# Kernel optimization log

Measured on AMD Instinct MI355X. Metric: run time of the kernel, lower is better.

The kernel has to match this reference:

```python
import jax, jax.numpy as jnp
import numpy as np

# ---- dims (mirror reconstructed HybridSignToTextModel) ----
INPUT_SIZE = 256
CONV_CH = 512
ENC_HID = 512          # per-direction encoder GRU hidden
ENC_OUT = 2 * ENC_HID  # bidirectional concat = 1024
DEC_LAYERS = 2
DEC_HID = 512
EMB = 512
VOCAB = 8000
ATTN = 512
MAX_DEC = 50
SOS, EOS, PAD = 1, 2, 0


def _gru_cell(x, h, Wih, Whh, bih, bhh):
    # torch GRUCell math. x:(B,I) h:(B,H) Wih:(3H,I) Whh:(3H,H)
    gi = x @ Wih.T + bih
    gh = h @ Whh.T + bhh
    H = h.shape[-1]
    ir, iz, inn = gi[:, :H], gi[:, H:2*H], gi[:, 2*H:]
    hr, hz, hn = gh[:, :H], gh[:, H:2*H], gh[:, 2*H:]
    r = jax.nn.sigmoid(ir + hr)
    z = jax.nn.sigmoid(iz + hz)
    n = jnp.tanh(inn + r * hn)
    return (1.0 - z) * n + z * h


def _gru_layer(xs, h0, Wih, Whh, bih, bhh, reverse=False):
    # xs: (T,B,I) -> outputs (T,B,H), final h (B,H)
    def step(h, x):
        h = _gru_cell(x, h, Wih, Whh, bih, bhh)
        return h, h
    hT, ys = jax.lax.scan(step, h0, xs, reverse=reverse)
    return ys, hT


def _conv1d(x, w, b, stride):
    # x:(B,C,T) w:(O,C,K) 'same'-ish padding K//2
    k = w.shape[-1]
    y = jax.lax.conv_general_dilated(x, w, (stride,), [(k // 2, k // 2)],
                                     dimension_numbers=("NCH", "OIH", "NCH"))
    return y + b[None, :, None]


def setup_inputs() -> dict:
    key = jax.random.key(0)
    ks = iter(jax.random.split(key, 40))
    def rn(shape, s=0.05):
        return (jax.random.normal(next(ks), shape, dtype=jnp.float32) * s)
    p = {}
    p["features"] = jax.random.normal(next(ks), (32, 512, INPUT_SIZE), dtype=jnp.float32)
    # conv encoder: 2 conv1d layers, stride 2 each, ReLU
    p["conv_w1"] = rn((CONV_CH, INPUT_SIZE, 5)); p["conv_b1"] = rn((CONV_CH,))
    p["conv_w2"] = rn((CONV_CH, CONV_CH, 5)); p["conv_b2"] = rn((CONV_CH,))
    # bidirectional encoder GRU (1 layer)
    for d in ("f", "b"):
        p[f"enc_Wih_{d}"] = rn((3 * ENC_HID, CONV_CH))
        p[f"enc_Whh_{d}"] = rn((3 * ENC_HID, ENC_HID))
        p[f"enc_bih_{d}"] = rn((3 * ENC_HID,))
        p[f"enc_bhh_{d}"] = rn((3 * ENC_HID,))
    # hidden bridge: 2*ENC_HID -> DEC_LAYERS*DEC_HID
    p["bridge_W"] = rn((DEC_LAYERS * DEC_HID, 2 * ENC_HID)); p["bridge_b"] = rn((DEC_LAYERS * DEC_HID,))
    # decoder embedding
    p["emb"] = rn((VOCAB, EMB), 0.1)
    # Bahdanau attention
    p["attn_We"] = rn((ATTN, ENC_OUT)); p["attn_Wd"] = rn((ATTN, DEC_HID)); p["attn_v"] = rn((ATTN,))
    # decoder GRU: 2 layers; layer0 in = EMB+ENC_OUT, layer1 in = DEC_HID
    ins = [EMB + ENC_OUT, DEC_HID]
    for l in range(DEC_LAYERS):
        p[f"dec_Wih{l}"] = rn((3 * DEC_HID, ins[l]))
        p[f"dec_Whh{l}"] = rn((3 * DEC_HID, DEC_HID))
        p[f"dec_bih{l}"] = rn((3 * DEC_HID,))
        p[f"dec_bhh{l}"] = rn((3 * DEC_HID,))
    # output proj: DEC_HID + ENC_OUT -> VOCAB
    p["proj_W"] = rn((VOCAB, DEC_HID + ENC_OUT)); p["proj_b"] = rn((VOCAB,))
    return p


def reference(features, conv_w1, conv_b1, conv_w2, conv_b2,
              enc_Wih_f, enc_Whh_f, enc_bih_f, enc_bhh_f,
              enc_Wih_b, enc_Whh_b, enc_bih_b, enc_bhh_b,
              bridge_W, bridge_b, emb, attn_We, attn_Wd, attn_v,
              dec_Wih0, dec_Whh0, dec_bih0, dec_bhh0,
              dec_Wih1, dec_Whh1, dec_bih1, dec_bhh1,
              proj_W, proj_b):
    B = features.shape[0]
    # ---- conv encoder ----
    x = features.transpose(0, 2, 1)                 # (B,C,T)
    x = jax.nn.relu(_conv1d(x, conv_w1, conv_b1, 2))
    x = jax.nn.relu(_conv1d(x, conv_w2, conv_b2, 2))
    x = x.transpose(2, 0, 1)                        # (T',B,C)
    # ---- bidirectional GRU encoder ----
    h0 = jnp.zeros((B, ENC_HID), features.dtype)
    yf, hf = _gru_layer(x, h0, enc_Wih_f, enc_Whh_f, enc_bih_f, enc_bhh_f)
    yb, hb = _gru_layer(x, h0, enc_Wih_b, enc_Whh_b, enc_bih_b, enc_bhh_b, reverse=True)
    enc_out = jnp.concatenate([yf, yb], -1).transpose(1, 0, 2)   # (B,T',2H)
    combined = jnp.concatenate([hf, hb], -1)                      # (B,2H)
    dec_h = (combined @ bridge_W.T + bridge_b).reshape(B, DEC_LAYERS, DEC_HID).transpose(1, 0, 2)
    # precompute attention keys
    enc_proj = jnp.einsum("bte,ae->bta", enc_out, attn_We)       # (B,T',A)

    def attention(h_top):
        score = jnp.einsum("bta,a->bt", jnp.tanh(enc_proj + (h_top @ attn_Wd.T)[:, None, :]), attn_v)
        w = jax.nn.softmax(score, axis=-1)
        return jnp.einsum("bt,bte->be", w, enc_out)               # (B,2H)

    def decode_step(carry, _):
        tok, h = carry                                            # h: (L,B,H)
        e = emb[tok]                                              # (B,EMB)
        ctx = attention(h[-1])
        g0 = _gru_cell(jnp.concatenate([e, ctx], -1), h[0], dec_Wih0, dec_Whh0, dec_bih0, dec_bhh0)
        g1 = _gru_cell(g0, h[1], dec_Wih1, dec_Whh1, dec_bih1, dec_bhh1)
        logits = jnp.concatenate([g1, ctx], -1) @ proj_W.T + proj_b
        nxt = jnp.argmax(logits, -1)
        return (nxt, jnp.stack([g0, g1])), nxt

    init_tok = jnp.full((B,), SOS, dtype=jnp.int32)
    _, toks = jax.lax.scan(decode_step, (init_tok, dec_h), None, length=MAX_DEC - 1)
    decoded = jnp.concatenate([init_tok[:, None], toks.T], axis=1)  # (B,MAX_DEC)
    return decoded
```

## Files before the change

### kernel.cpp

```cpp
#include <hip/hip_runtime.h>
#include <math.h>

#define DINLINE __device__ __forceinline__

DINLINE float sigmoidf_(float x) { return 1.f / (1.f + expf(-x)); }

__device__ __align__(256) float g_ws[36200000];

__global__ void im2col1_kernel(const float* __restrict__ feat, float* __restrict__ P) {
  size_t i = (size_t)blockIdx.x * 256 + threadIdx.x;
  int col = (int)(i % 1280);
  int row = (int)(i / 1280);
  int c = col / 5, k = col - c * 5;
  int l = row & 255, b = row >> 8;
  int pos = 2 * l + k - 2;
  P[i] = (pos >= 0 && pos < 512) ? feat[((size_t)b * 512 + pos) * 256 + c] : 0.f;
}

__global__ void im2col2_kernel(const float* __restrict__ y1, float* __restrict__ P) {
  size_t i = (size_t)blockIdx.x * 256 + threadIdx.x;
  int col = (int)(i % 2560);
  int row = (int)(i / 2560);
  int c = col / 5, k = col - c * 5;
  int l = row & 127, b = row >> 7;
  int pos = 2 * l + k - 2;
  P[i] = (pos >= 0 && pos < 256) ? y1[((size_t)b * 256 + pos) * 512 + c] : 0.f;
}

__global__ __launch_bounds__(256) void sgemm128(
    const float* __restrict__ A, const float* __restrict__ B,
    const float* __restrict__ bias, float* __restrict__ C,
    int M, int N, int K, int relu) {
  __shared__ float As[8][132];
  __shared__ float Bs[8][132];
  int bm = blockIdx.y * 128, bn = blockIdx.x * 128;
  int tid = threadIdx.x;
  int tx = tid & 15, ty = tid >> 4;
  float acc[8][8];
#pragma unroll
  for (int i = 0; i < 8; ++i)
#pragma unroll
    for (int j = 0; j < 8; ++j) acc[i][j] = 0.f;
  int lr = tid >> 1;
  int lc = (tid & 1) * 4;
  const float* Arow = A + (size_t)(bm + lr) * K + lc;
  const float* Brow = B + (size_t)(bn + lr) * K + lc;
  for (int k0 = 0; k0 < K; k0 += 8) {
    float4 av = *(const float4*)(Arow + k0);
    float4 bv = *(const float4*)(Brow + k0);
    As[lc + 0][lr] = av.x; As[lc + 1][lr] = av.y; As[lc + 2][lr] = av.z; As[lc + 3][lr] = av.w;
    Bs[lc + 0][lr] = bv.x; Bs[lc + 1][lr] = bv.y; Bs[lc + 2][lr] = bv.z; Bs[lc + 3][lr] = bv.w;
    __syncthreads();
#pragma unroll
    for (int kk = 0; kk < 8; ++kk) {
      float4 a0 = *(const float4*)&As[kk][ty * 8];
      float4 a1 = *(const float4*)&As[kk][ty * 8 + 4];
      float4 b0 = *(const float4*)&Bs[kk][tx * 8];
      float4 b1 = *(const float4*)&Bs[kk][tx * 8 + 4];
      float aa[8] = {a0.x, a0.y, a0.z, a0.w, a1.x, a1.y, a1.z, a1.w};
      float bb[8] = {b0.x, b0.y, b0.z, b0.w, b1.x, b1.y, b1.z, b1.w};
#pragma unroll
      for (int i = 0; i < 8; ++i)
#pragma unroll
        for (int j = 0; j < 8; ++j) acc[i][j] += aa[i] * bb[j];
    }
    __syncthreads();
  }
#pragma unroll
  for (int i = 0; i < 8; ++i) {
    int m = bm + ty * 8 + i;
#pragma unroll
    for (int j = 0; j < 8; ++j) {
      int n = bn + tx * 8 + j;
      float v = acc[i][j] + (bias ? bias[n] : 0.f);
      if (relu) v = fmaxf(v, 0.f);
      C[(size_t)m * N + n] = v;
    }
  }
}

__global__ __launch_bounds__(256) void enc_gru_step(
    const float* __restrict__ gi_f, const float* __restrict__ gi_b,
    const float* __restrict__ Whh_f, const float* __restrict__ bhh_f,
    const float* __restrict__ Whh_b, const float* __restrict__ bhh_b,
    const float* __restrict__ h_in, float* __restrict__ h_out,
    float* __restrict__ enc_out, int s) {
  int dir = blockIdx.x >> 6;
  int j = ((blockIdx.x & 63) << 3) + (threadIdx.x >> 5);
  int b = threadIdx.x & 31;
  __shared__ float4 hs4[32 * 128];
  const float4* hbase = (const float4*)(h_in + dir * 32 * 512);
  for (int i = threadIdx.x; i < 32 * 128; i += 256) {
    int bb = i >> 7, kf = i & 127;
    hs4[bb * 128 + (kf ^ (bb & 7))] = hbase[i];
  }
  __syncthreads();
  const float* gi = dir ? gi_b : gi_f;
  const float* Whh = dir ? Whh_b : Whh_f;
  const float* bhh = dir ? bhh_b : bhh_f;
  int t = dir ? (127 - s) : s;
  const float4* wr = (const float4*)(Whh + (size_t)j * 512);
  const float4* wz = (const float4*)(Whh + (size_t)(512 + j) * 512);
  const float4* wn = (const float4*)(Whh + (size_t)(1024 + j) * 512);
  const float4* hrow = hs4 + b * 128;
  int sw = b & 7;
  float sr = 0.f, sz = 0.f, sn = 0.f;
#pragma unroll 4
  for (int kf = 0; kf < 128; ++kf) {
    float4 hv = hrow[kf ^ sw];
    float4 r4 = wr[kf];
    float4 z4 = wz[kf];
    float4 n4 = wn[kf];
    sr += hv.x * r4.x + hv.y * r4.y + hv.z * r4.z + hv.w * r4.w;
    sz += hv.x * z4.x + hv.y * z4.y + hv.z * z4.z + hv.w * z4.w;
    sn += hv.x * n4.x + hv.y * n4.y + hv.z * n4.z + hv.w * n4.w;
  }
  const float* g = gi + ((size_t)b * 128 + t) * 1536;
  float r = sigmoidf_(g[j] + sr + bhh[j]);
  float z = sigmoidf_(g[512 + j] + sz + bhh[512 + j]);
  float n = tanhf(g[1024 + j] + r * (sn + bhh[1024 + j]));
  float4 hj4 = hrow[(j >> 2) ^ sw];
  float hj = ((const float*)&hj4)[j & 3];
  float hnew = (1.f - z) * n + z * hj;
  h_out[dir * 32 * 512 + b * 512 + j] = hnew;
  enc_out[((size_t)b * 128 + t) * 1024 + dir * 512 + j] = hnew;
}

__global__ __launch_bounds__(256) void dec_gru_step(
    const float* __restrict__ gi, const float* __restrict__ Whh,
    const float* __restrict__ bhh,
    const float* __restrict__ h_in, float* __restrict__ h_out) {
  int j = (blockIdx.x << 3) + (threadIdx.x >> 5);
  int b = threadIdx.x & 31;
  __shared__ float4 hs4[32 * 128];
  const float4* hbase = (const float4*)h_in;
  for (int i = threadIdx.x; i < 32 * 128; i += 256) {
    int bb = i >> 7, kf = i & 127;
    hs4[bb * 128 + (kf ^ (bb & 7))] = hbase[i];
  }
  __syncthreads();
  const float4* wr = (const float4*)(Whh + (size_t)j * 512);
  const float4* wz = (const float4*)(Whh + (size_t)(512 + j) * 512);
  const float4* wn = (const float4*)(Whh + (size_t)(1024 + j) * 512);
  const float4* hrow = hs4 + b * 128;
  int sw = b & 7;
  float sr = 0.f, sz = 0.f, sn = 0.f;
#pragma unroll 4
  for (int kf = 0; kf < 128; ++kf) {
    float4 hv = hrow[kf ^ sw];
    float4 r4 = wr[kf];
    float4 z4 = wz[kf];
    float4 n4 = wn[kf];
    sr += hv.x * r4.x + hv.y * r4.y + hv.z * r4.z + hv.w * r4.w;
    sz += hv.x * z4.x + hv.y * z4.y + hv.z * z4.z + hv.w * z4.w;
    sn += hv.x * n4.x + hv.y * n4.y + hv.z * n4.z + hv.w * n4.w;
  }
  const float* g = gi + (size_t)b * 1536;
  float r = sigmoidf_(g[j] + sr + bhh[j]);
  float z = sigmoidf_(g[512 + j] + sz + bhh[512 + j]);
  float n = tanhf(g[1024 + j] + r * (sn + bhh[1024 + j]));
  float4 hj4 = hrow[(j >> 2) ^ sw];
  float hj = ((const float*)&hj4)[j & 3];
  h_out[b * 512 + j] = (1.f - z) * n + z * hj;
}

__global__ __launch_bounds__(256) void gemvB(
    const float* __restrict__ A1, const int* __restrict__ tokidx, int len1,
    const float* __restrict__ A2, int len2,
    const float* __restrict__ W, const float* __restrict__ bias,
    float* __restrict__ out0, float* __restrict__ out1, int split, int N, int K) {
  int tid = threadIdx.x;
  int s = tid & 7, nl = tid >> 3;
  int n = blockIdx.x * 32 + nl;
  __shared__ float4 xs4[32 * 32];
  float acc[32];
#pragma unroll
  for (int b = 0; b < 32; ++b) acc[b] = 0.f;
  const float4* W4 = (const float4*)(W + (size_t)n * K);
  int K4 = K >> 2;
  int len1_4 = len1 >> 2;
  for (int k0 = 0; k0 < K4; k0 += 32) {
    __syncthreads();
    for (int idx = tid; idx < 1024; idx += 256) {
      int b = idx >> 5, kf = idx & 31;
      int gk = k0 + kf;
      float4 v;
      if (gk < len1_4) {
        const float* src = tokidx ? (A1 + (size_t)tokidx[b] * len1) : (A1 + (size_t)b * len1);
        v = ((const float4*)src)[gk];
      } else {
        v = ((const float4*)(A2 + (size_t)b * len2))[gk - len1_4];
      }
      xs4[idx] = v;
    }
    __syncthreads();
    const float4* wp = W4 + k0;
#pragma unroll
    for (int j = 0; j < 4; ++j) {
      float4 wv = wp[j * 8 + s];
      const float4* xp = xs4 + j * 8 + s;
#pragma unroll
      for (int b = 0; b < 32; ++b) {
        float4 xv = xp[b * 32];
        acc[b] += wv.x * xv.x + wv.y * xv.y + wv.z * xv.z + wv.w * xv.w;
      }
    }
  }
#pragma unroll
  for (int b = 0; b < 32; ++b) {
    float v = acc[b];
    v += __shfl_xor(v, 1);
    v += __shfl_xor(v, 2);
    v += __shfl_xor(v, 4);
    acc[b] = v;
  }
  if (s == 0) {
    float bv = bias ? bias[n] : 0.f;
#pragma unroll
    for (int b = 0; b < 32; ++b) {
      float val = acc[b] + bv;
      if (n < split) out0[(size_t)b * split + n] = val;
      else out1[(size_t)b * (N - split) + (n - split)] = val;
    }
  }
}

__global__ __launch_bounds__(512) void attention_kernel(
    const float* __restrict__ dbuf,
    const float* __restrict__ v,
    const float* __restrict__ enc_proj,
    const float* __restrict__ enc_out,
    float* __restrict__ ctx) {
  int b = blockIdx.x;
  int tid = threadIdx.x;
  __shared__ float d[512];
  __shared__ float red[512];
  __shared__ float sc[128];
  d[tid] = dbuf[b * 512 + tid];
  __syncthreads();
  {
    int t = tid >> 2, part = tid & 3;
    const float* ep = enc_proj + ((size_t)b * 128 + t) * 512 + part * 128;
    const float* dd = d + part * 128;
    const float* vv = v + part * 128;
    float s = 0.f;
    for (int a = 0; a < 128; ++a) s += tanhf(ep[a] + dd[a]) * vv[a];
    red[tid] = s;
  }
  __syncthreads();
  if (tid < 128) sc[tid] = red[tid * 4] + red[tid * 4 + 1] + red[tid * 4 + 2] + red[tid * 4 + 3];
  __syncthreads();
  if (tid == 0) {
    float m = -1e30f;
    for (int t = 0; t < 128; ++t) m = fmaxf(m, sc[t]);
    float sum = 0.f;
    for (int t = 0; t < 128; ++t) { float e = expf(sc[t] - m); sc[t] = e; sum += e; }
    float inv = 1.f / sum;
    for (int t = 0; t < 128; ++t) sc[t] *= inv;
  }
  __syncthreads();
  for (int e = tid; e < 1024; e += 512) {
    const float* eo = enc_out + (size_t)b * 131072 + e;
    float s = 0.f;
    for (int t = 0; t < 128; ++t) s += sc[t] * eo[(size_t)t * 1024];
    ctx[b * 1024 + e] = s;
  }
}

__global__ __launch_bounds__(256) void argmax_kernel(
    const float* __restrict__ logits, int* __restrict__ tok,
    int* __restrict__ decoded, int step) {
  int b = blockIdx.x, tid = threadIdx.x;
  __shared__ float bv[256];
  __shared__ int bi[256];
  float best = -3.4e38f;
  int bidx = 0x7fffffff;
  const float* L = logits + (size_t)b * 8000;
  for (int v = tid; v < 8000; v += 256) {
    float x = L[v];
    if (x > best) { best = x; bidx = v; }
  }
  bv[tid] = best; bi[tid] = bidx;
  __syncthreads();
  for (int s = 128; s > 0; s >>= 1) {
    if (tid < s) {
      if (bv[tid + s] > bv[tid] || (bv[tid + s] == bv[tid] && bi[tid + s] < bi[tid])) {
        bv[tid] = bv[tid + s];
        bi[tid] = bi[tid + s];
      }
    }
    __syncthreads();
  }
  if (tid == 0) { tok[b] = bi[0]; decoded[b * 50 + step + 1] = bi[0]; }
}

__global__ void init_kernel(int* __restrict__ tok, int* __restrict__ decoded) {
  int b = threadIdx.x;
  if (b >= 32) return;
  tok[b] = 1;
  decoded[b * 50] = 1;
}

__global__ void zero_kernel(float* __restrict__ p, int n) {
  int i = blockIdx.x * 256 + threadIdx.x;
  if (i < n) p[i] = 0.f;
}

extern "C" void kernel_launch(void* const* d_in, const int* in_sizes, int n_in,
                              void* d_out, int out_size, void* d_ws, size_t ws_size,
                              hipStream_t stream) {
  const float* features  = (const float*)d_in[0];
  const float* conv_w1   = (const float*)d_in[1];
  const float* conv_b1   = (const float*)d_in[2];
  const float* conv_w2   = (const float*)d_in[3];
  const float* conv_b2   = (const float*)d_in[4];
  const float* enc_Wih_f = (const float*)d_in[5];
  const float* enc_Whh_f = (const float*)d_in[6];
  const float* enc_bih_f = (const float*)d_in[7];
  const float* enc_bhh_f = (const float*)d_in[8];
  const float* enc_Wih_b = (const float*)d_in[9];
  const float* enc_Whh_b = (const float*)d_in[10];
  const float* enc_bih_b = (const float*)d_in[11];
  const float* enc_bhh_b = (const float*)d_in[12];
  const float* bridge_W  = (const float*)d_in[13];
  const float* bridge_b  = (const float*)d_in[14];
  const float* emb       = (const float*)d_in[15];
  const float* attn_We   = (const float*)d_in[16];
  const float* attn_Wd   = (const float*)d_in[17];
  const float* attn_v    = (const float*)d_in[18];
  const float* dec_Wih0  = (const float*)d_in[19];
  const float* dec_Whh0  = (const float*)d_in[20];
  const float* dec_bih0  = (const float*)d_in[21];
  const float* dec_bhh0  = (const float*)d_in[22];
  const float* dec_Wih1  = (const float*)d_in[23];
  const float* dec_Whh1  = (const float*)d_in[24];
  const float* dec_bih1  = (const float*)d_in[25];
  const float* dec_bhh1  = (const float*)d_in[26];
  const float* proj_W    = (const float*)d_in[27];
  const float* proj_b    = (const float*)d_in[28];
  int* decoded = (int*)d_out;

  float* ws = nullptr;
  hipGetSymbolAddress((void**)&ws, HIP_SYMBOL(g_ws));
  float* P       = ws;
  float* y1      = ws + 10485760;
  float* x2      = ws + 14680064;
  float* gi_f    = ws + 16777216;
  float* gi_b    = ws + 23068672;
  float* enc_out = ws + 29360128;
  float* enc_pj  = ws + 33554432;
  float* h_enc   = ws + 35651584;
  float* h0d     = ws + 35717120;
  float* h1d     = ws + 35749888;
  float* ctxb    = ws + 35782656;
  float* gi0     = ws + 35815424;
  float* gi1     = ws + 35864576;
  float* logits  = ws + 35913728;
  float* dbuf    = ws + 36169728;
  int*   tok     = (int*)(ws + 36186112);

  im2col1_kernel<<<40960, 256, 0, stream>>>(features, P);
  sgemm128<<<dim3(4, 64), 256, 0, stream>>>(P, conv_w1, conv_b1, y1, 8192, 512, 1280, 1);
  im2col2_kernel<<<40960, 256, 0, stream>>>(y1, P);
  sgemm128<<<dim3(4, 32), 256, 0, stream>>>(P, conv_w2, conv_b2, x2, 4096, 512, 2560, 1);

  sgemm128<<<dim3(12, 32), 256, 0, stream>>>(x2, enc_Wih_f, enc_bih_f, gi_f, 4096, 1536, 512, 0);
  sgemm128<<<dim3(12, 32), 256, 0, stream>>>(x2, enc_Wih_b, enc_bih_b, gi_b, 4096, 1536, 512, 0);

  zero_kernel<<<256, 256, 0, stream>>>(h_enc, 65536);
  for (int s = 0; s < 128; ++s) {
    enc_gru_step<<<128, 256, 0, stream>>>(gi_f, gi_b,
        enc_Whh_f, enc_bhh_f, enc_Whh_b, enc_bhh_b,
        h_enc + (s & 1) * 32768, h_enc + ((s + 1) & 1) * 32768, enc_out, s);
  }
  float* h_fin = h_enc;

  gemvB<<<32, 256, 0, stream>>>(h_fin, nullptr, 512, h_fin + 16384, 512,
      bridge_W, bridge_b, h0d, h1d, 512, 1024, 1024);

  sgemm128<<<dim3(4, 32), 256, 0, stream>>>(enc_out, attn_We, nullptr, enc_pj, 4096, 512, 1024, 0);

  init_kernel<<<1, 64, 0, stream>>>(tok, decoded);

  for (int s = 0; s < 49; ++s) {
    int cur = s & 1, nxt = (s + 1) & 1;
    gemvB<<<16, 256, 0, stream>>>(h1d + cur * 16384, nullptr, 512, nullptr, 0,
        attn_Wd, nullptr, dbuf, nullptr, 512, 512, 512);
    attention_kernel<<<32, 512, 0, stream>>>(dbuf, attn_v, enc_pj, enc_out, ctxb);
    gemvB<<<48, 256, 0, stream>>>(emb, tok, 512, ctxb, 1024,
        dec_Wih0, dec_bih0, gi0, nullptr, 1536, 1536, 1536);
    dec_gru_step<<<64, 256, 0, stream>>>(gi0, dec_Whh0, dec_bhh0,
        h0d + cur * 16384, h0d + nxt * 16384);
    gemvB<<<48, 256, 0, stream>>>(h0d + nxt * 16384, nullptr, 512, nullptr, 0,
        dec_Wih1, dec_bih1, gi1, nullptr, 1536, 1536, 512);
    dec_gru_step<<<64, 256, 0, stream>>>(gi1, dec_Whh1, dec_bhh1,
        h1d + cur * 16384, h1d + nxt * 16384);
    gemvB<<<250, 256, 0, stream>>>(h1d + nxt * 16384, nullptr, 512, ctxb, 1024,
        proj_W, proj_b, logits, nullptr, 8000, 8000, 1536);
    argmax_kernel<<<32, 256, 0, stream>>>(logits, tok, decoded, s);
  }
}
```

Measured before the change: 18.91 ms.

## Fuse decoder step kernels: attention+query GEMV, GRU input+hidden, proj+argmax

The decoder loop goes from eight kernels per step to four. The attention query GEMV moves into the attention kernel, each GRU layer computes its input and hidden projections in one kernel, and the vocabulary projection does the argmax itself with packed 64-bit atomicMax keys. The previous token is decoded at the start of the next step, and a final kernel writes the last token. The aim is to cut launch overhead and intermediate global-memory round trips. The encoder GRU step also moves to 128-thread blocks, which doubles the block count and the number of shared-memory h reloads. Risks are fewer blocks for the input-projection GEMV, since 64 blocks now each stream the full Wih rows, and sensitivity to tie-breaking in the argmax key ordering.

```diff
diff --git a/kernel.cpp b/kernel.cpp
--- a/kernel.cpp
+++ b/kernel.cpp
@@ -79,20 +79,20 @@
   }
 }
 
-__global__ __launch_bounds__(256) void enc_gru_step(
+__global__ __launch_bounds__(128) void enc_gru_step(
     const float* __restrict__ gi_f, const float* __restrict__ gi_b,
     const float* __restrict__ Whh_f, const float* __restrict__ bhh_f,
     const float* __restrict__ Whh_b, const float* __restrict__ bhh_b,
     const float* __restrict__ h_in, float* __restrict__ h_out,
     float* __restrict__ enc_out, int s) {
-  int dir = blockIdx.x >> 6;
-  int j = ((blockIdx.x & 63) << 3) + (threadIdx.x >> 5);
+  int dir = blockIdx.x >> 7;
+  int j = ((blockIdx.x & 127) << 2) + (threadIdx.x >> 5);
   int b = threadIdx.x & 31;
-  __shared__ float4 hs4[32 * 128];
+  __shared__ float4 hs4[4096];
   const float4* hbase = (const float4*)(h_in + dir * 32 * 512);
-  for (int i = threadIdx.x; i < 32 * 128; i += 256) {
+  for (int i = threadIdx.x; i < 4096; i += 128) {
     int bb = i >> 7, kf = i & 127;
-    hs4[bb * 128 + (kf ^ (bb & 7))] = hbase[i];
+    hs4[(bb << 7) + (kf ^ (bb & 7))] = hbase[i];
   }
   __syncthreads();
   const float* gi = dir ? gi_b : gi_f;
@@ -126,39 +126,80 @@
   enc_out[((size_t)b * 128 + t) * 1024 + dir * 512 + j] = hnew;
 }
 
-__global__ __launch_bounds__(256) void dec_gru_step(
-    const float* __restrict__ gi, const float* __restrict__ Whh,
-    const float* __restrict__ bhh,
-    const float* __restrict__ h_in, float* __restrict__ h_out) {
-  int j = (blockIdx.x << 3) + (threadIdx.x >> 5);
-  int b = threadIdx.x & 31;
-  __shared__ float4 hs4[32 * 128];
+__global__ __launch_bounds__(256) void dec_gru_fused(
+    const float* __restrict__ A1, const int* __restrict__ tokidx, int len1,
+    const float* __restrict__ A2, int len2,
+    const float* __restrict__ Wih, const float* __restrict__ bih,
+    const float* __restrict__ Whh, const float* __restrict__ bhh,
+    const float* __restrict__ h_in, float* __restrict__ h_out,
+    unsigned long long* __restrict__ keys_zero) {
+  __shared__ float4 buf[4096];
+  int tid = threadIdx.x;
+  int b = tid & 31, j = (blockIdx.x << 3) + (tid >> 5);
+  if (keys_zero && blockIdx.x == 0 && tid < 32) keys_zero[tid] = 0ULL;
+  int Kin = len1 + len2;
+  const float4* wir = (const float4*)(Wih + (size_t)j * Kin);
+  const float4* wiz = (const float4*)(Wih + (size_t)(512 + j) * Kin);
+  const float4* win = (const float4*)(Wih + (size_t)(1024 + j) * Kin);
+  int K4 = Kin >> 2, len1_4 = len1 >> 2;
+  float gr = 0.f, gz = 0.f, gn = 0.f;
+  int sw5 = b & 31;
+  for (int k0 = 0; k0 < K4; k0 += 32) {
+    __syncthreads();
+    for (int idx = tid; idx < 1024; idx += 256) {
+      int bb = idx >> 5, kf = idx & 31;
+      int gk = k0 + kf;
+      float4 v;
+      if (gk < len1_4) {
+        const float* src = tokidx ? (A1 + (size_t)tokidx[bb] * len1) : (A1 + (size_t)bb * len1);
+        v = ((const float4*)src)[gk];
+      } else {
+        v = ((const float4*)(A2 + (size_t)bb * len2))[gk - len1_4];
+      }
+      buf[(bb << 5) + (kf ^ (bb & 31))] = v;
+    }
+    __syncthreads();
+    const float4* xrow = buf + (b << 5);
+    const float4* wr_ = wir + k0;
+    const float4* wz_ = wiz + k0;
+    const float4* wn_ = win + k0;
+#pragma unroll 4
+    for (int kf = 0; kf < 32; ++kf) {
+      float4 xv = xrow[kf ^ sw5];
+      float4 r4 = wr_[kf];
+      float4 z4 = wz_[kf];
+      float4 n4 = wn_[kf];
+      gr += xv.x * r4.x + xv.y * r4.y + xv.z * r4.z + xv.w * r4.w;
+      gz += xv.x * z4.x + xv.y * z4.y + xv.z * z4.z + xv.w * z4.w;
+      gn += xv.x * n4.x + xv.y * n4.y + xv.z * n4.z + xv.w * n4.w;
+    }
+  }
+  __syncthreads();
   const float4* hbase = (const float4*)h_in;
-  for (int i = threadIdx.x; i < 32 * 128; i += 256) {
+  for (int i = tid; i < 4096; i += 256) {
     int bb = i >> 7, kf = i & 127;
-    hs4[bb * 128 + (kf ^ (bb & 7))] = hbase[i];
-  }
-  __syncthreads();
-  const float4* wr = (const float4*)(Whh + (size_t)j * 512);
-  const float4* wz = (const float4*)(Whh + (size_t)(512 + j) * 512);
-  const float4* wn = (const float4*)(Whh + (size_t)(1024 + j) * 512);
-  const float4* hrow = hs4 + b * 128;
+    buf[(bb << 7) + (kf ^ (bb & 7))] = hbase[i];
+  }
+  __syncthreads();
+  const float4* whr = (const float4*)(Whh + (size_t)j * 512);
+  const float4* whz = (const float4*)(Whh + (size_t)(512 + j) * 512);
+  const float4* whn = (const float4*)(Whh + (size_t)(1024 + j) * 512);
+  const float4* hrow = buf + (b << 7);
   int sw = b & 7;
   float sr = 0.f, sz = 0.f, sn = 0.f;
 #pragma unroll 4
   for (int kf = 0; kf < 128; ++kf) {
     float4 hv = hrow[kf ^ sw];
-    float4 r4 = wr[kf];
-    float4 z4 = wz[kf];
-    float4 n4 = wn[kf];
+    float4 r4 = whr[kf];
+    float4 z4 = whz[kf];
+    float4 n4 = whn[kf];
     sr += hv.x * r4.x + hv.y * r4.y + hv.z * r4.z + hv.w * r4.w;
     sz += hv.x * z4.x + hv.y * z4.y + hv.z * z4.z + hv.w * z4.w;
     sn += hv.x * n4.x + hv.y * n4.y + hv.z * n4.z + hv.w * n4.w;
   }
-  const float* g = gi + (size_t)b * 1536;
-  float r = sigmoidf_(g[j] + sr + bhh[j]);
-  float z = sigmoidf_(g[512 + j] + sz + bhh[512 + j]);
-  float n = tanhf(g[1024 + j] + r * (sn + bhh[1024 + j]));
+  float r = sigmoidf_(gr + bih[j] + sr + bhh[j]);
+  float z = sigmoidf_(gz + bih[512 + j] + sz + bhh[512 + j]);
+  float n = tanhf(gn + bih[1024 + j] + r * (sn + bhh[1024 + j]));
   float4 hj4 = hrow[(j >> 2) ^ sw];
   float hj = ((const float*)&hj4)[j & 3];
   h_out[b * 512 + j] = (1.f - z) * n + z * hj;
@@ -225,18 +266,109 @@
   }
 }
 
-__global__ __launch_bounds__(512) void attention_kernel(
-    const float* __restrict__ dbuf,
+__global__ __launch_bounds__(256) void proj_argmax_kernel(
+    const float* __restrict__ A1, int len1,
+    const float* __restrict__ A2, int len2,
+    const float* __restrict__ W, const float* __restrict__ bias,
+    unsigned long long* __restrict__ keys) {
+  int tid = threadIdx.x;
+  int s = tid & 7, nl = tid >> 3;
+  int n = blockIdx.x * 32 + nl;
+  __shared__ float4 xs4[32 * 32];
+  __shared__ unsigned long long ksh[32][33];
+  float acc[32];
+#pragma unroll
+  for (int b = 0; b < 32; ++b) acc[b] = 0.f;
+  int K = len1 + len2;
+  const float4* W4 = (const float4*)(W + (size_t)n * K);
+  int K4 = K >> 2;
+  int len1_4 = len1 >> 2;
+  for (int k0 = 0; k0 < K4; k0 += 32) {
+    __syncthreads();
+    for (int idx = tid; idx < 1024; idx += 256) {
+      int b = idx >> 5, kf = idx & 31;
+      int gk = k0 + kf;
+      float4 v;
+      if (gk < len1_4) v = ((const float4*)(A1 + (size_t)b * len1))[gk];
+      else v = ((const float4*)(A2 + (size_t)b * len2))[gk - len1_4];
+      xs4[idx] = v;
+    }
+    __syncthreads();
+    const float4* wp = W4 + k0;
+#pragma unroll
+    for (int j = 0; j < 4; ++j) {
+      float4 wv = wp[j * 8 + s];
+      const float4* xp = xs4 + j * 8 + s;
+#pragma unroll
+      for (int b = 0; b < 32; ++b) {
+        float4 xv = xp[b * 32];
+        acc[b] += wv.x * xv.x + wv.y * xv.y + wv.z * xv.z + wv.w * xv.w;
+      }
+    }
+  }
+#pragma unroll
+  for (int b = 0; b < 32; ++b) {
+    float v = acc[b];
+    v += __shfl_xor(v, 1);
+    v += __shfl_xor(v, 2);
+    v += __shfl_xor(v, 4);
+    acc[b] = v;
+  }
+  if (s == 0) {
+    float bv = bias[n];
+#pragma unroll
+    for (int b = 0; b < 32; ++b) {
+      float val = acc[b] + bv;
+      unsigned u = __float_as_uint(val);
+      u = (u & 0x80000000u) ? ~u : (u | 0x80000000u);
+      ksh[nl][b] = ((unsigned long long)u << 32) | (unsigned long long)(0xFFFFFFFFu - (unsigned)n);
+    }
+  }
+  __syncthreads();
+  if (tid < 32) {
+    unsigned long long best = 0ULL;
+#pragma unroll 8
+    for (int q = 0; q < 32; ++q) {
+      unsigned long long v = ksh[q][tid];
+      if (v > best) best = v;
+    }
+    atomicMax(&keys[tid], best);
+  }
+}
+
+__global__ __launch_bounds__(512) void attn_fused(
+    const float* __restrict__ h1,
+    const float* __restrict__ Wd,
     const float* __restrict__ v,
     const float* __restrict__ enc_proj,
     const float* __restrict__ enc_out,
-    float* __restrict__ ctx) {
+    float* __restrict__ ctx,
+    const unsigned long long* __restrict__ keys,
+    int* __restrict__ tok, int* __restrict__ decoded, int step) {
   int b = blockIdx.x;
   int tid = threadIdx.x;
+  if (step > 0 && b == 0 && tid < 32) {
+    unsigned long long k = keys[tid];
+    int n = (int)(0xFFFFFFFFu - (unsigned)(k & 0xFFFFFFFFull));
+    tok[tid] = n;
+    decoded[tid * 50 + step] = n;
+  }
+  __shared__ float hs[512];
   __shared__ float d[512];
   __shared__ float red[512];
   __shared__ float sc[128];
-  d[tid] = dbuf[b * 512 + tid];
+  hs[tid] = h1[b * 512 + tid];
+  __syncthreads();
+  {
+    const float* w = Wd + (size_t)tid * 512;
+    float s = 0.f;
+    for (int k = 0; k < 512; k += 4) {
+      float4 wv = *(const float4*)&w[k];
+      float4 hv = *(const float4*)&hs[k];
+      s += hv.x * wv.x + hv.y * wv.y + hv.z * wv.z + hv.w * wv.w;
+    }
+    d[tid] = s;
+  }
   __syncthreads();
   {
     int t = tid >> 2, part = tid & 3;
@@ -267,31 +399,12 @@
   }
 }
 
-__global__ __launch_bounds__(256) void argmax_kernel(
-    const float* __restrict__ logits, int* __restrict__ tok,
-    int* __restrict__ decoded, int step) {
-  int b = blockIdx.x, tid = threadIdx.x;
-  __shared__ float bv[256];
-  __shared__ int bi[256];
-  float best = -3.4e38f;
-  int bidx = 0x7fffffff;
-  const float* L = logits + (size_t)b * 8000;
-  for (int v = tid; v < 8000; v += 256) {
-    float x = L[v];
-    if (x > best) { best = x; bidx = v; }
-  }
-  bv[tid] = best; bi[tid] = bidx;
-  __syncthreads();
-  for (int s = 128; s > 0; s >>= 1) {
-    if (tid < s) {
-      if (bv[tid + s] > bv[tid] || (bv[tid + s] == bv[tid] && bi[tid + s] < bi[tid])) {
-        bv[tid] = bv[tid + s];
-        bi[tid] = bi[tid + s];
-      }
-    }
-    __syncthreads();
-  }
-  if (tid == 0) { tok[b] = bi[0]; decoded[b * 50 + step + 1] = bi[0]; }
+__global__ void final_tok_kernel(const unsigned long long* __restrict__ keys,
+                                 int* __restrict__ decoded) {
+  int b = threadIdx.x;
+  if (b >= 32) return;
+  int n = (int)(0xFFFFFFFFu - (unsigned)(keys[b] & 0xFFFFFFFFull));
+  decoded[b * 50 + 49] = n;
 }
 
 __global__ void init_kernel(int* __restrict__ tok, int* __restrict__ decoded) {
@@ -353,11 +466,8 @@
   float* h0d     = ws + 35717120;
   float* h1d     = ws + 35749888;
   float* ctxb    = ws + 35782656;
-  float* gi0     = ws + 35815424;
-  float* gi1     = ws + 35864576;
-  float* logits  = ws + 35913728;
-  float* dbuf    = ws + 36169728;
-  int*   tok     = (int*)(ws + 36186112);
+  unsigned long long* keys = (unsigned long long*)(ws + 35815424);
+  int*   tok     = (int*)(ws + 35815488);
 
   im2col1_kernel<<<40960, 256, 0, stream>>>(features, P);
   sgemm128<<<dim3(4, 64), 256, 0, stream>>>(P, conv_w1, conv_b1, y1, 8192, 512, 1280, 1);
@@ -369,7 +479,7 @@
 
   zero_kernel<<<256, 256, 0, stream>>>(h_enc, 65536);
   for (int s = 0; s < 128; ++s) {
-    enc_gru_step<<<128, 256, 0, stream>>>(gi_f, gi_b,
+    enc_gru_step<<<256, 128, 0, stream>>>(gi_f, gi_b,
         enc_Whh_f, enc_bhh_f, enc_Whh_b, enc_bhh_b,
         h_enc + (s & 1) * 32768, h_enc + ((s + 1) & 1) * 32768, enc_out, s);
   }
@@ -384,19 +494,16 @@
 
   for (int s = 0; s < 49; ++s) {
     int cur = s & 1, nxt = (s + 1) & 1;
-    gemvB<<<16, 256, 0, stream>>>(h1d + cur * 16384, nullptr, 512, nullptr, 0,
-        attn_Wd, nullptr, dbuf, nullptr, 512, 512, 512);
-    attention_kernel<<<32, 512, 0, stream>>>(dbuf, attn_v, enc_pj, enc_out, ctxb);
-    gemvB<<<48, 256, 0, stream>>>(emb, tok, 512, ctxb, 1024,
-        dec_Wih0, dec_bih0, gi0, nullptr, 1536, 1536, 1536);
-    dec_gru_step<<<64, 256, 0, stream>>>(gi0, dec_Whh0, dec_bhh0,
-        h0d + cur * 16384, h0d + nxt * 16384);
-    gemvB<<<48, 256, 0, stream>>>(h0d + nxt * 16384, nullptr, 512, nullptr, 0,
-        dec_Wih1, dec_bih1, gi1, nullptr, 1536, 1536, 512);
-    dec_gru_step<<<64, 256, 0, stream>>>(gi1, dec_Whh1, dec_bhh1,
-        h1d + cur * 16384, h1d + nxt * 16384);
-    gemvB<<<250, 256, 0, stream>>>(h1d + nxt * 16384, nullptr, 512, ctxb, 1024,
-        proj_W, proj_b, logits, nullptr, 8000, 8000, 1536);
-    argmax_kernel<<<32, 256, 0, stream>>>(logits, tok, decoded, s);
-  }
-}
+    attn_fused<<<32, 512, 0, stream>>>(h1d + cur * 16384, attn_Wd, attn_v,
+                                       enc_pj, enc_out, ctxb, keys, tok, decoded, s);
+    dec_gru_fused<<<64, 256, 0, stream>>>(emb, tok, 512, ctxb, 1024,
+        dec_Wih0, dec_bih0, dec_Whh0, dec_bhh0,
+        h0d + cur * 16384, h0d + nxt * 16384, nullptr);
+    dec_gru_fused<<<64, 256, 0, stream>>>(h0d + nxt * 16384, nullptr, 512, nullptr, 0,
+        dec_Wih1, dec_bih1, dec_Whh1, dec_bhh1,
+        h1d + cur * 16384, h1d + nxt * 16384, keys);
+    proj_argmax_kernel<<<250, 256, 0, stream>>>(h1d + nxt * 16384, 512, ctxb, 1024,
+        proj_W, proj_b, keys);
+  }
+  final_tok_kernel<<<1, 32, 0, stream>>>(keys, decoded);
+}
```

Result: slower. 19.93 ms (+5.4%).
